# Kernel optimization log

Measured on AMD Instinct MI355X. Metric: run time of the kernel, lower is better.

The kernel has to match this reference:

```python
import jax, jax.numpy as jnp
import numpy as np
import math

EMBED_DIM = 1024
NUM_HEADS = 16
HEAD_DIM = EMBED_DIM // NUM_HEADS
B, S = 4, 2048


def setup_inputs() -> dict:
    key = jax.random.key(0)
    ks = jax.random.split(key, 12)
    sc = 1.0 / math.sqrt(EMBED_DIM)
    inp = {
        'query': jax.random.normal(ks[0], (B, S, EMBED_DIM), jnp.float32),
        'key': jax.random.normal(ks[1], (B, S, EMBED_DIM), jnp.float32),
        'value': jax.random.normal(ks[2], (B, S, EMBED_DIM), jnp.float32),
        # causal mask: 1 = attend, 0 = masked (matches masked_fill(attn_mask == 0, -inf))
        'attn_mask': jnp.tril(jnp.ones((S, S), jnp.int32)),
        'Wq': jax.random.normal(ks[3], (EMBED_DIM, EMBED_DIM), jnp.float32) * sc,
        'bq': jax.random.normal(ks[4], (EMBED_DIM,), jnp.float32) * sc,
        'Wk': jax.random.normal(ks[5], (EMBED_DIM, EMBED_DIM), jnp.float32) * sc,
        'bk': jax.random.normal(ks[6], (EMBED_DIM,), jnp.float32) * sc,
        'Wv': jax.random.normal(ks[7], (EMBED_DIM, EMBED_DIM), jnp.float32) * sc,
        'bv': jax.random.normal(ks[8], (EMBED_DIM,), jnp.float32) * sc,
        'Wo': jax.random.normal(ks[9], (EMBED_DIM, EMBED_DIM), jnp.float32) * sc,
        'bo': jax.random.normal(ks[10], (EMBED_DIM,), jnp.float32) * sc,
    }
    return inp


def reference(query, key, value, attn_mask, Wq, bq, Wk, bk, Wv, bv, Wo, bo):
    b, s, _ = query.shape
    # torch nn.Linear: x @ W.T + b
    q = (query @ Wq.T + bq).reshape(b, s, NUM_HEADS, HEAD_DIM)
    k = (key @ Wk.T + bk).reshape(b, s, NUM_HEADS, HEAD_DIM)
    v = (value @ Wv.T + bv).reshape(b, s, NUM_HEADS, HEAD_DIM)
    scores = jnp.einsum('bqhd,bkhd->bhqk', q, k) / math.sqrt(HEAD_DIM)
    neg_inf = jnp.asarray(-jnp.inf, scores.dtype)
    scores = jnp.where(attn_mask[None, None, :, :] == 0, neg_inf, scores)
    attn = jax.nn.softmax(scores, axis=-1)
    # dropout is identity in eval mode
    out = jnp.einsum('bhqk,bkhd->bqhd', attn, v).reshape(b, s, EMBED_DIM)
    return out @ Wo.T + bo
```

## Files before the change

kernel.cpp:

```cpp
#include <hip/hip_runtime.h>
#include <math.h>


#define EMBED 1024
#define SEQ   2048
#define NH    16
#define HD    64
#define QSCALE 0.18033688011112042f

typedef __attribute__((ext_vector_type(4))) float f32x4;
typedef __attribute__((ext_vector_type(8))) short s16x8;
typedef __attribute__((ext_vector_type(4))) short s16x4;
typedef __attribute__((ext_vector_type(4))) unsigned int u32x4;
typedef __attribute__((ext_vector_type(2))) unsigned int u32x2;

#define GLDS16(gp, lp) __builtin_amdgcn_global_load_lds( \
    (const __attribute__((address_space(1))) void*)(gp), \
    (__attribute__((address_space(3))) void*)(lp), 16, 0, 0)

__device__ __forceinline__ unsigned short f2bf(float f) {
    unsigned int u = __builtin_bit_cast(unsigned int, f);
    u += 0x7fffu + ((u >> 16) & 1u);
    return (unsigned short)(u >> 16);
}
__device__ __forceinline__ unsigned int pkbf(float lo, float hi) {
    return __builtin_amdgcn_perm(__builtin_bit_cast(unsigned int, hi),
                                 __builtin_bit_cast(unsigned int, lo),
                                 0x07060302u);
}

struct CvtArgs { const float* s[4]; unsigned short* d[4]; };
__global__ void cvt_w(CvtArgs ca)
{
    const float* in = ca.s[blockIdx.y];
    unsigned short* out = ca.d[blockIdx.y];
    int i = blockIdx.x * 256 + threadIdx.x;
    f32x4 v = *(const f32x4*)(in + (size_t)i * 4);
    s16x4 p;
    p[0] = (short)f2bf(v[0]); p[1] = (short)f2bf(v[1]);
    p[2] = (short)f2bf(v[2]); p[3] = (short)f2bf(v[3]);
    *(s16x4*)(out + (size_t)i * 4) = p;
}

struct ProjArgs {
    const float* X[3];
    const unsigned short* W[3];
    const float* Bz[3];
    unsigned short* Oz[3];
};
__global__ void __launch_bounds__(256)
gemm_qkv(ProjArgs pa)
{
    __shared__ float Af[128 * 64];
    __shared__ unsigned short Bb[128 * 64];
    const int z = blockIdx.z;
    const float* X = pa.X[z];
    const unsigned short* Wb = pa.W[z];
    const float* bias = pa.Bz[z];
    unsigned short* Out = pa.Oz[z];
    const float scale = (z == 0) ? QSCALE : 1.0f;
    const int tid = threadIdx.x, lane = tid & 63, wv = tid >> 6;
    const int g = lane >> 4, c = lane & 15;
    const int wx = wv & 1, wy = wv >> 1;
    const int bm0 = blockIdx.x * 128, bn0 = blockIdx.y * 128;

    f32x4 acc[4][4];
#pragma unroll
    for (int i = 0; i < 4; ++i)
#pragma unroll
        for (int n = 0; n < 4; ++n) acc[i][n] = f32x4{0.f, 0.f, 0.f, 0.f};

    for (int k0 = 0; k0 < EMBED; k0 += 64) {
        __syncthreads();
#pragma unroll
        for (int cc = 0; cc < 8; ++cc) {
            int li = cc * 256 + tid;
            int row = li >> 4, ch = (li & 15) ^ (row & 15);
            GLDS16(X + (size_t)(bm0 + row) * EMBED + k0 + ch * 4,
                   Af + cc * 1024 + wv * 256);
        }
#pragma unroll
        for (int cc = 0; cc < 4; ++cc) {
            int li = cc * 256 + tid;
            int row = li >> 3, ch = (li & 7) ^ (row & 7);
            GLDS16(Wb + (size_t)(bn0 + row) * EMBED + k0 + ch * 8,
                   Bb + cc * 2048 + wv * 512);
        }
        __syncthreads();
#pragma unroll
        for (int ks = 0; ks < 2; ++ks) {
            const int ia0 = ((ks * 8 + g * 2) ^ c) * 4;
            const int ia1 = ((ks * 8 + g * 2 + 1) ^ c) * 4;
            const int ib  = ((ks * 4 + g) ^ (c & 7)) * 8;
            s16x8 af[4], bfr[4];
#pragma unroll
            for (int i = 0; i < 4; ++i) {
                const float* ap = &Af[(wy * 64 + i * 16 + c) * 64];
                f32x4 a0 = *(const f32x4*)(ap + ia0);
                f32x4 a1 = *(const f32x4*)(ap + ia1);
                u32x4 t;
                t[0] = pkbf(a0[0], a0[1]); t[1] = pkbf(a0[2], a0[3]);
                t[2] = pkbf(a1[0], a1[1]); t[3] = pkbf(a1[2], a1[3]);
                af[i] = __builtin_bit_cast(s16x8, t);
            }
#pragma unroll
            for (int n = 0; n < 4; ++n)
                bfr[n] = *(const s16x8*)(&Bb[(wx * 64 + n * 16 + c) * 64 + ib]);
#pragma unroll
            for (int i = 0; i < 4; ++i)
#pragma unroll
                for (int n = 0; n < 4; ++n)
                    acc[i][n] = __builtin_amdgcn_mfma_f32_16x16x32_bf16(af[i], bfr[n], acc[i][n], 0, 0, 0);
        }
    }
    if (z < 2) {
#pragma unroll
        for (int i = 0; i < 4; ++i) {
            int m0 = bm0 + wy * 64 + i * 16 + g * 4;
            int bb = m0 >> 11, s0 = m0 & 2047;
#pragma unroll
            for (int n = 0; n < 4; ++n) {
                int ncol = bn0 + wx * 64 + n * 16 + c;
                float bv = bias[ncol];
                int hh = ncol >> 6, dd = ncol & 63;
                size_t base = (((size_t)bb * NH + hh) * SEQ + s0) * HD + dd;
#pragma unroll
                for (int r = 0; r < 4; ++r)
                    Out[base + (size_t)r * HD] = f2bf((acc[i][n][r] + bv) * scale);
            }
        }
    } else {
#pragma unroll
        for (int i = 0; i < 4; ++i) {
            int m0 = bm0 + wy * 64 + i * 16 + g * 4;
            int bb = m0 >> 11, s0 = m0 & 2047;
#pragma unroll
            for (int n = 0; n < 4; ++n) {
                int ncol = bn0 + wx * 64 + n * 16 + c;
                float bv = bias[ncol];
                int hh = ncol >> 6, dd = ncol & 63;
                s16x4 pk;
#pragma unroll
                for (int r = 0; r < 4; ++r) pk[r] = (short)f2bf(acc[i][n][r] + bv);
                *(s16x4*)(&Out[(((size_t)bb * NH + hh) * HD + dd) * SEQ + s0]) = pk;
            }
        }
    }
}

__global__ void __launch_bounds__(256)
gemm_out(const unsigned short* __restrict__ Xb, const unsigned short* __restrict__ Wb,
         const float* __restrict__ bias, float* __restrict__ Out)
{
    __shared__ unsigned short Ab[128 * 64];
    __shared__ unsigned short Bb[128 * 64];
    const int tid = threadIdx.x;
    const int lane = tid & 63, wv = tid >> 6;
    const int g = lane >> 4, c = lane & 15;
    const int wx = wv & 1, wy = wv >> 1;
    const int bm0 = blockIdx.x * 128, bn0 = blockIdx.y * 128;

    f32x4 acc[4][4];
#pragma unroll
    for (int i = 0; i < 4; ++i)
#pragma unroll
        for (int n = 0; n < 4; ++n) acc[i][n] = f32x4{0.f, 0.f, 0.f, 0.f};

    for (int k0 = 0; k0 < EMBED; k0 += 64) {
        __syncthreads();
#pragma unroll
        for (int cc = 0; cc < 4; ++cc) {
            int li = cc * 256 + tid;
            int row = li >> 3, ch = (li & 7) ^ (row & 7);
            GLDS16(Xb + (size_t)(bm0 + row) * EMBED + k0 + ch * 8,
                   Ab + cc * 2048 + wv * 512);
        }
#pragma unroll
        for (int cc = 0; cc < 4; ++cc) {
            int li = cc * 256 + tid;
            int row = li >> 3, ch = (li & 7) ^ (row & 7);
            GLDS16(Wb + (size_t)(bn0 + row) * EMBED + k0 + ch * 8,
                   Bb + cc * 2048 + wv * 512);
        }
        __syncthreads();
#pragma unroll
        for (int ks = 0; ks < 2; ++ks) {
            const int ib = ((ks * 4 + g) ^ (c & 7)) * 8;
            s16x8 af[4], bfr[4];
#pragma unroll
            for (int i = 0; i < 4; ++i)
                af[i] = *(const s16x8*)(&Ab[(wy * 64 + i * 16 + c) * 64 + ib]);
#pragma unroll
            for (int n = 0; n < 4; ++n)
                bfr[n] = *(const s16x8*)(&Bb[(wx * 64 + n * 16 + c) * 64 + ib]);
#pragma unroll
            for (int i = 0; i < 4; ++i)
#pragma unroll
                for (int n = 0; n < 4; ++n)
                    acc[i][n] = __builtin_amdgcn_mfma_f32_16x16x32_bf16(af[i], bfr[n], acc[i][n], 0, 0, 0);
        }
    }
#pragma unroll
    for (int i = 0; i < 4; ++i) {
#pragma unroll
        for (int n = 0; n < 4; ++n) {
            int ncol = bn0 + wx * 64 + n * 16 + c;
            float bv = bias[ncol];
#pragma unroll
            for (int r = 0; r < 4; ++r) {
                int m = bm0 + wy * 64 + i * 16 + g * 4 + r;
                Out[(size_t)m * EMBED + ncol] = acc[i][n][r] + bv;
            }
        }
    }
}

__global__ void __launch_bounds__(256)
attn_fwd(const unsigned short* __restrict__ Qb, const unsigned short* __restrict__ Kb,
         const unsigned short* __restrict__ Vg, unsigned short* __restrict__ Ob)
{
    __shared__ unsigned short Kt[64 * 64];
    __shared__ unsigned short Vt[64 * 64];
    __shared__ unsigned int   Pb[4][16 * 36];
    const int tid = threadIdx.x, lane = tid & 63, wv = tid >> 6;
    const int g = lane >> 4, c = lane & 15;
    const int h = blockIdx.y, b = blockIdx.z;
    const size_t bh = (size_t)b * NH + h;
    const unsigned short* K0 = Kb + bh * SEQ * HD;
    const unsigned short* V0 = Vg + bh * HD * SEQ;
    unsigned int* Pw = &Pb[wv][0];
    const int x0 = (g ^ (c & 7)) * 8;
    const int x1 = ((4 + g) ^ (c & 7)) * 8;

    for (int part = 0; part < 2; ++part) {
        const int qt = part ? blockIdx.x : (SEQ / 64 - 1 - blockIdx.x);
        const unsigned short* Qp = Qb + (bh * SEQ + qt * 64 + wv * 16) * HD;
        s16x8 qf0 = *(const s16x8*)(Qp + c * HD + g * 8);
        s16x8 qf1 = *(const s16x8*)(Qp + c * HD + 32 + g * 8);
        f32x4 o[4];
#pragma unroll
        for (int dt = 0; dt < 4; ++dt) o[dt] = f32x4{0.f, 0.f, 0.f, 0.f};
        float m_run = -INFINITY, l_run = 0.f;

        for (int kt = 0; kt <= qt; ++kt) {
            __syncthreads();
            {
                const unsigned short* Kg = K0 + (size_t)kt * 64 * HD;
#pragma unroll
                for (int cc = 0; cc < 2; ++cc) {
                    int li = cc * 256 + tid;
                    int row = li >> 3, ch = (li & 7) ^ (row & 7);
                    GLDS16(Kg + row * HD + ch * 8, Kt + cc * 2048 + wv * 512);
                }
#pragma unroll
                for (int cc = 0; cc < 2; ++cc) {
                    int li = cc * 256 + tid;
                    int row = li >> 3, ch = (li & 7) ^ (row & 7);
                    GLDS16(V0 + (size_t)row * SEQ + kt * 64 + ch * 8,
                           Vt + cc * 2048 + wv * 512);
                }
            }
            __syncthreads();

            const int ntmax = (kt == qt) ? wv : 3;
            f32x4 sc[4];
#pragma unroll
            for (int nt = 0; nt < 4; ++nt) {
                if (nt <= ntmax) {
                    f32x4 a = f32x4{0.f, 0.f, 0.f, 0.f};
                    s16x8 kf0 = *(const s16x8*)(&Kt[(nt * 16 + c) * 64 + x0]);
                    s16x8 kf1 = *(const s16x8*)(&Kt[(nt * 16 + c) * 64 + x1]);
                    a = __builtin_amdgcn_mfma_f32_16x16x32_bf16(kf0, qf0, a, 0, 0, 0);
                    a = __builtin_amdgcn_mfma_f32_16x16x32_bf16(kf1, qf1, a, 0, 0, 0);
                    sc[nt] = a;
                } else {
                    sc[nt] = f32x4{-INFINITY, -INFINITY, -INFINITY, -INFINITY};
                }
            }
            if (kt == qt) {
#pragma unroll
                for (int nt = 0; nt < 4; ++nt)
#pragma unroll
                    for (int r = 0; r < 4; ++r)
                        if (nt * 16 + g * 4 + r > wv * 16 + c) sc[nt][r] = -INFINITY;
            }
            float mloc = -INFINITY;
#pragma unroll
            for (int nt = 0; nt < 4; ++nt)
                mloc = fmaxf(mloc, fmaxf(fmaxf(sc[nt][0], sc[nt][1]),
                                         fmaxf(sc[nt][2], sc[nt][3])));
            mloc = fmaxf(mloc, __shfl_xor(mloc, 16));
            mloc = fmaxf(mloc, __shfl_xor(mloc, 32));
            float mnew = fmaxf(m_run, mloc);
            float alpha = exp2f(m_run - mnew);
            float rs = 0.f;
#pragma unroll
            for (int nt = 0; nt < 4; ++nt)
#pragma unroll
                for (int r = 0; r < 4; ++r) {
                    float p = exp2f(sc[nt][r] - mnew);
                    sc[nt][r] = p;
                    rs += p;
                }
            rs += __shfl_xor(rs, 16);
            rs += __shfl_xor(rs, 32);
            l_run = l_run * alpha + rs;
            m_run = mnew;
            float av[4];
#pragma unroll
            for (int r = 0; r < 4; ++r) av[r] = __shfl(alpha, g * 4 + r, 16);
#pragma unroll
            for (int dt = 0; dt < 4; ++dt)
#pragma unroll
                for (int r = 0; r < 4; ++r) o[dt][r] *= av[r];
#pragma unroll
            for (int nt = 0; nt < 4; ++nt) {
                u32x2 w;
                w[0] = pkbf(sc[nt][0], sc[nt][1]);
                w[1] = pkbf(sc[nt][2], sc[nt][3]);
                *(u32x2*)(&Pw[c * 36 + nt * 8 + g * 2]) = w;
            }
#pragma unroll
            for (int kc = 0; kc < 2; ++kc) {
                s16x8 pf = *(const s16x8*)(&Pw[c * 36 + kc * 16 + g * 4]);
                const int xv = kc ? x1 : x0;
#pragma unroll
                for (int dt = 0; dt < 4; ++dt) {
                    s16x8 vf = *(const s16x8*)(&Vt[(dt * 16 + c) * 64 + xv]);
                    o[dt] = __builtin_amdgcn_mfma_f32_16x16x32_bf16(pf, vf, o[dt], 0, 0, 0);
                }
            }
        }
        float linv = 1.0f / l_run;
        float lv[4];
#pragma unroll
        for (int r = 0; r < 4; ++r) lv[r] = __shfl(linv, g * 4 + r, 16);
#pragma unroll
        for (int r = 0; r < 4; ++r) {
            int srow = qt * 64 + wv * 16 + g * 4 + r;
            size_t base = ((size_t)b * SEQ + srow) * EMBED + h * HD;
#pragma unroll
            for (int dt = 0; dt < 4; ++dt)
                Ob[base + dt * 16 + c] = f2bf(o[dt][r] * lv[r]);
        }
    }
}

extern "C" void kernel_launch(void* const* d_in, const int* in_sizes, int n_in,
                              void* d_out, int out_size, void* d_ws, size_t ws_size,
                              hipStream_t stream)
{
    (void)in_sizes; (void)n_in; (void)out_size; (void)ws_size;
    const float* Xq = (const float*)d_in[0];
    const float* Xk = (const float*)d_in[1];
    const float* Xv = (const float*)d_in[2];
    const float* Wq = (const float*)d_in[4];
    const float* bq = (const float*)d_in[5];
    const float* Wk = (const float*)d_in[6];
    const float* bk = (const float*)d_in[7];
    const float* Wv = (const float*)d_in[8];
    const float* bv = (const float*)d_in[9];
    const float* Wo = (const float*)d_in[10];
    const float* bo = (const float*)d_in[11];
    float* Out = (float*)d_out;

    unsigned short* ws = (unsigned short*)d_ws;
    unsigned short* wqb = ws;
    unsigned short* wkb = wqb + 1048576;
    unsigned short* wvb = wkb + 1048576;
    unsigned short* wob = wvb + 1048576;
    unsigned short* Qb  = wob + 1048576;
    unsigned short* Kb  = Qb + 8388608;
    unsigned short* Vb  = Kb + 8388608;
    unsigned short* Ax  = Vb + 8388608;

    CvtArgs ca;
    ca.s[0] = Wq; ca.s[1] = Wk; ca.s[2] = Wv; ca.s[3] = Wo;
    ca.d[0] = wqb; ca.d[1] = wkb; ca.d[2] = wvb; ca.d[3] = wob;
    cvt_w<<<dim3(1024, 4), 256, 0, stream>>>(ca);

    ProjArgs pa;
    pa.X[0] = Xq; pa.X[1] = Xk; pa.X[2] = Xv;
    pa.W[0] = wqb; pa.W[1] = wkb; pa.W[2] = wvb;
    pa.Bz[0] = bq; pa.Bz[1] = bk; pa.Bz[2] = bv;
    pa.Oz[0] = Qb; pa.Oz[1] = Kb; pa.Oz[2] = Vb;
    gemm_qkv<<<dim3(64, 8, 3), 256, 0, stream>>>(pa);

    attn_fwd<<<dim3(16, NH, 4), 256, 0, stream>>>(Qb, Kb, Vb, Ax);

    gemm_out<<<dim3(64, 8), 256, 0, stream>>>(Ax, wob, bo, Out);
}
```

Before: 361.2 us.

## Double-buffer K/V tiles in attention and skip redundant softmax rescaling

The attention kernel now keeps two LDS buffers each for K and V. It prefetches the next key tile with global_load_lds while computing on the current one, which cuts the two barriers per iteration down to one and overlaps global loads with the MFMA and softmax work. The online-softmax rescale of the output accumulators and the running sum now runs only when some row's max actually increases (checked with a wave-wide __any). exp2f is replaced by the hardware exp2 intrinsic. The cost is doubled LDS use for K/V, which may reduce occupancy, plus a slightly less precise exp.

```diff
diff --git a/kernel.cpp b/kernel.cpp
--- a/kernel.cpp
+++ b/kernel.cpp
@@ -219,8 +219,8 @@
 attn_fwd(const unsigned short* __restrict__ Qb, const unsigned short* __restrict__ Kb,
          const unsigned short* __restrict__ Vg, unsigned short* __restrict__ Ob)
 {
-    __shared__ unsigned short Kt[64 * 64];
-    __shared__ unsigned short Vt[64 * 64];
+    __shared__ unsigned short Kt[2][64 * 64];
+    __shared__ unsigned short Vt[2][64 * 64];
     __shared__ unsigned int   Pb[4][16 * 36];
     const int tid = threadIdx.x, lane = tid & 63, wv = tid >> 6;
     const int g = lane >> 4, c = lane & 15;
@@ -231,6 +231,11 @@
     unsigned int* Pw = &Pb[wv][0];
     const int x0 = (g ^ (c & 7)) * 8;
     const int x1 = ((4 + g) ^ (c & 7)) * 8;
+    const int li0 = tid, li1 = 256 + tid;
+    const int kr0 = (li0 >> 3) * HD + (((li0 & 7) ^ ((li0 >> 3) & 7)) << 3);
+    const int kr1 = (li1 >> 3) * HD + (((li1 & 7) ^ ((li1 >> 3) & 7)) << 3);
+    const int vr0 = (li0 >> 3) * SEQ + (((li0 & 7) ^ ((li0 >> 3) & 7)) << 3);
+    const int vr1 = (li1 >> 3) * SEQ + (((li1 & 7) ^ ((li1 >> 3) & 7)) << 3);
 
     for (int part = 0; part < 2; ++part) {
         const int qt = part ? blockIdx.x : (SEQ / 64 - 1 - blockIdx.x);
@@ -242,25 +247,29 @@
         for (int dt = 0; dt < 4; ++dt) o[dt] = f32x4{0.f, 0.f, 0.f, 0.f};
         float m_run = -INFINITY, l_run = 0.f;
 
+        __syncthreads();
+        {
+            const unsigned short* Kg = K0;
+            GLDS16(Kg + kr0, &Kt[0][0] + wv * 512);
+            GLDS16(Kg + kr1, &Kt[0][2048] + wv * 512);
+            GLDS16(V0 + vr0, &Vt[0][0] + wv * 512);
+            GLDS16(V0 + vr1, &Vt[0][2048] + wv * 512);
+        }
+
         for (int kt = 0; kt <= qt; ++kt) {
             __syncthreads();
-            {
-                const unsigned short* Kg = K0 + (size_t)kt * 64 * HD;
-#pragma unroll
-                for (int cc = 0; cc < 2; ++cc) {
-                    int li = cc * 256 + tid;
-                    int row = li >> 3, ch = (li & 7) ^ (row & 7);
-                    GLDS16(Kg + row * HD + ch * 8, Kt + cc * 2048 + wv * 512);
-                }
-#pragma unroll
-                for (int cc = 0; cc < 2; ++cc) {
-                    int li = cc * 256 + tid;
-                    int row = li >> 3, ch = (li & 7) ^ (row & 7);
-                    GLDS16(V0 + (size_t)row * SEQ + kt * 64 + ch * 8,
-                           Vt + cc * 2048 + wv * 512);
-                }
-            }
-            __syncthreads();
+            const int cur = kt & 1;
+            if (kt < qt) {
+                const int nxt = cur ^ 1;
+                const unsigned short* Kg = K0 + (size_t)(kt + 1) * 64 * HD;
+                GLDS16(Kg + kr0, &Kt[nxt][0] + wv * 512);
+                GLDS16(Kg + kr1, &Kt[nxt][2048] + wv * 512);
+                const unsigned short* Vp = V0 + (kt + 1) * 64;
+                GLDS16(Vp + vr0, &Vt[nxt][0] + wv * 512);
+                GLDS16(Vp + vr1, &Vt[nxt][2048] + wv * 512);
+            }
+            const unsigned short* Kc = &Kt[cur][0];
+            const unsigned short* Vc = &Vt[cur][0];
 
             const int ntmax = (kt == qt) ? wv : 3;
             f32x4 sc[4];
@@ -268,8 +277,8 @@
             for (int nt = 0; nt < 4; ++nt) {
                 if (nt <= ntmax) {
                     f32x4 a = f32x4{0.f, 0.f, 0.f, 0.f};
-                    s16x8 kf0 = *(const s16x8*)(&Kt[(nt * 16 + c) * 64 + x0]);
-                    s16x8 kf1 = *(const s16x8*)(&Kt[(nt * 16 + c) * 64 + x1]);
+                    s16x8 kf0 = *(const s16x8*)(&Kc[(nt * 16 + c) * 64 + x0]);
+                    s16x8 kf1 = *(const s16x8*)(&Kc[(nt * 16 + c) * 64 + x1]);
                     a = __builtin_amdgcn_mfma_f32_16x16x32_bf16(kf0, qf0, a, 0, 0, 0);
                     a = __builtin_amdgcn_mfma_f32_16x16x32_bf16(kf1, qf1, a, 0, 0, 0);
                     sc[nt] = a;
@@ -291,28 +300,31 @@
                                          fmaxf(sc[nt][2], sc[nt][3])));
             mloc = fmaxf(mloc, __shfl_xor(mloc, 16));
             mloc = fmaxf(mloc, __shfl_xor(mloc, 32));
-            float mnew = fmaxf(m_run, mloc);
-            float alpha = exp2f(m_run - mnew);
+            if (__any(mloc > m_run)) {
+                float mnew = fmaxf(m_run, mloc);
+                float alpha = __builtin_amdgcn_exp2f(m_run - mnew);
+                m_run = mnew;
+                l_run *= alpha;
+                float av[4];
+#pragma unroll
+                for (int r = 0; r < 4; ++r) av[r] = __shfl(alpha, g * 4 + r, 16);
+#pragma unroll
+                for (int dt = 0; dt < 4; ++dt)
+#pragma unroll
+                    for (int r = 0; r < 4; ++r) o[dt][r] *= av[r];
+            }
             float rs = 0.f;
 #pragma unroll
             for (int nt = 0; nt < 4; ++nt)
 #pragma unroll
                 for (int r = 0; r < 4; ++r) {
-                    float p = exp2f(sc[nt][r] - mnew);
+                    float p = __builtin_amdgcn_exp2f(sc[nt][r] - m_run);
                     sc[nt][r] = p;
                     rs += p;
                 }
             rs += __shfl_xor(rs, 16);
             rs += __shfl_xor(rs, 32);
-            l_run = l_run * alpha + rs;
-            m_run = mnew;
-            float av[4];
-#pragma unroll
-            for (int r = 0; r < 4; ++r) av[r] = __shfl(alpha, g * 4 + r, 16);
-#pragma unroll
-            for (int dt = 0; dt < 4; ++dt)
-#pragma unroll
-                for (int r = 0; r < 4; ++r) o[dt][r] *= av[r];
+            l_run += rs;
 #pragma unroll
             for (int nt = 0; nt < 4; ++nt) {
                 u32x2 w;
@@ -326,7 +338,7 @@
                 const int xv = kc ? x1 : x0;
 #pragma unroll
                 for (int dt = 0; dt < 4; ++dt) {
-                    s16x8 vf = *(const s16x8*)(&Vt[(dt * 16 + c) * 64 + xv]);
+                    s16x8 vf = *(const s16x8*)(&Vc[(dt * 16 + c) * 64 + xv]);
                     o[dt] = __builtin_amdgcn_mfma_f32_16x16x32_bf16(pf, vf, o[dt], 0, 0, 0);
                 }
             }
```

New measurement: 350.9 us. 2.8% less time.
